# Performance work log

Hardware: AMD Instinct MI355X
Metric: run time of the kernel (lower is better)

Reference implementation:

```python
import jax, jax.numpy as jnp
import numpy as np
import math

B, N, HID, NH = 128, 512, 512, 8
DH = HID // NH  # d_heads = 64


def setup_inputs() -> dict:
    key = jax.random.key(0)
    ks = jax.random.split(key, 8)
    s = 0.05  # keep logits in a sane range
    h = jax.random.normal(ks[0], (B, N, HID), dtype=jnp.float32)
    lengths = jax.random.randint(ks[1], (B,), 1, N + 1, dtype=jnp.int32)
    w_q = jax.random.normal(ks[2], (HID, HID), dtype=jnp.float32) * s
    w_k = jax.random.normal(ks[3], (HID, HID), dtype=jnp.float32) * s
    w_v = jax.random.normal(ks[4], (HID, HID), dtype=jnp.float32) * s
    w_o = jax.random.normal(ks[5], (HID, HID), dtype=jnp.float32) * s
    w_seed_w = jax.random.normal(ks[6], (HID, 1), dtype=jnp.float32) * s  # Linear(1, k*hidden), k=1
    w_seed_b = jax.random.normal(ks[7], (HID,), dtype=jnp.float32) * s
    seed_vec = jnp.ones((1,), dtype=jnp.float32)
    return {"h": h, "lengths": lengths, "w_q": w_q, "w_k": w_k, "w_v": w_v,
            "w_o": w_o, "w_seed_w": w_seed_w, "w_seed_b": w_seed_b, "seed_vec": seed_vec}


def reference(h, lengths, w_q, w_k, w_v, w_o, w_seed_w, w_seed_b, seed_vec):
    # PMA with k=1 seed query. norm_features=False.
    # query = w_seed(seed_vec), same for every graph in the batch.
    query = w_seed_w @ seed_vec + w_seed_b            # [HID]
    q = (w_q @ query).reshape(NH, DH)                 # [NH, DH] (Linear: x @ W.T == W @ x for vector)
    # NOTE: original code computes w_k(v) but never uses it in attention; output
    # depends only on q and v (e = q * v summed over d_heads). We skip the dead compute.
    v = (h @ w_v.T).reshape(B, N, NH, DH)             # [B, N, NH, DH]
    # logits: e[b,h,n] = <q[h], v[b,n,h]> / sqrt(DH)
    e = jnp.einsum("hd,bnhd->bhn", q, v) / math.sqrt(DH)
    valid = jnp.arange(N)[None, :] < lengths[:, None]  # [B, N] ragged mask
    e = jnp.where(valid[:, None, :], e, -jnp.inf)
    alpha = jax.nn.softmax(e, axis=-1)                # [B, NH, N]; padded cols -> 0
    out_h = jnp.einsum("bhn,bnhd->bhd", alpha, v)     # [B, NH, DH]
    out = out_h.reshape(B, HID) @ w_o.T               # [B*k, HID], packed (k=1)
    alpha_out = alpha[..., None]                      # [B, NH, N, 1] matching torch permute
    return out, alpha_out
```

## Files before the change

### kernel.cpp

```cpp
#include <hip/hip_runtime.h>
#include <math.h>

constexpr int B = 128, N = 512, HID = 512, NH = 8, DH = 64;

__global__ __launch_bounds__(64) void k1_qk(
    const float* __restrict__ w_q, const float* __restrict__ w_v,
    const float* __restrict__ w_sw, const float* __restrict__ w_sb,
    const float* __restrict__ seed, float* __restrict__ qk)
{
    __shared__ __align__(16) float query_s[HID];
    __shared__ float q_s[DH];
    const int t  = threadIdx.x;
    const int h  = blockIdx.x >> 3;
    const int jc = blockIdx.x & 7;
    const float sv = seed[0];
    #pragma unroll
    for (int k = 0; k < 8; ++k) {
        const int j = t * 8 + k;
        query_s[j] = w_sw[j] * sv + w_sb[j];
    }
    __syncthreads();
    {
        const float* row = w_q + (size_t)(h * DH + t) * HID;
        float acc = 0.f;
        for (int j = 0; j < HID; j += 4) {
            const float4 wv = *(const float4*)(row + j);
            acc += wv.x * query_s[j]     + wv.y * query_s[j + 1]
                 + wv.z * query_s[j + 2] + wv.w * query_s[j + 3];
        }
        q_s[t] = acc;
    }
    __syncthreads();
    {
        const int j = jc * 64 + t;
        float acc = 0.f;
        for (int d = 0; d < DH; ++d)
            acc += q_s[d] * w_v[(size_t)(h * DH + d) * HID + j];
        qk[h * HID + j] = acc * 0.125f;
    }
}

__global__ __launch_bounds__(256) void ke_logits(
    const float* __restrict__ hbuf, const int* __restrict__ lengths,
    const float* __restrict__ qk, float* __restrict__ e_ws)
{
    const int t = threadIdx.x;
    const int l = t & 63;
    const int w = t >> 6;
    const int b = blockIdx.x >> 3;
    const int c = blockIdx.x & 7;
    const int n0 = c * 64;
    const int len = lengths[b];
    if (n0 >= len) return;

    float4 qlo[NH], qhi[NH];
    #pragma unroll
    for (int hh = 0; hh < NH; ++hh) {
        qlo[hh] = *(const float4*)&qk[hh * HID + l * 4];
        qhi[hh] = *(const float4*)&qk[hh * HID + 256 + l * 4];
    }

    const int nmax = min(n0 + 64, len);
    const float* hb = hbuf + (size_t)b * N * HID;
    const int hh_out = ((l & 1) << 2) | (l & 2) | ((l >> 2) & 1);

    for (int n = n0 + w; n < nmax; n += 4) {
        const float* row = hb + (size_t)n * HID;
        const float4 h0 = *(const float4*)(row + l * 4);
        const float4 h1 = *(const float4*)(row + 256 + l * 4);
        float v[NH];
        #pragma unroll
        for (int hh = 0; hh < NH; ++hh)
            v[hh] = h0.x * qlo[hh].x + h0.y * qlo[hh].y
                  + h0.z * qlo[hh].z + h0.w * qlo[hh].w
                  + h1.x * qhi[hh].x + h1.y * qhi[hh].y
                  + h1.z * qhi[hh].z + h1.w * qhi[hh].w;

        #pragma unroll
        for (int i = 0; i < 4; ++i) {
            const float ax = __shfl_xor(v[i], 1, 64);
            const float bx = __shfl_xor(v[i + 4], 1, 64);
            v[i] = (l & 1) ? (v[i + 4] + bx) : (v[i] + ax);
        }
        #pragma unroll
        for (int i = 0; i < 2; ++i) {
            const float ax = __shfl_xor(v[i], 2, 64);
            const float bx = __shfl_xor(v[i + 2], 2, 64);
            v[i] = (l & 2) ? (v[i + 2] + bx) : (v[i] + ax);
        }
        {
            const float ax = __shfl_xor(v[0], 4, 64);
            const float bx = __shfl_xor(v[1], 4, 64);
            v[0] = (l & 4) ? (v[1] + bx) : (v[0] + ax);
        }
        v[0] += __shfl_xor(v[0], 8, 64);
        v[0] += __shfl_xor(v[0], 16, 64);
        v[0] += __shfl_xor(v[0], 32, 64);

        if (l < 8)
            e_ws[(size_t)(b * NH + hh_out) * N + n] = v[0];
    }
}

__global__ __launch_bounds__(256) void ks_softmax(
    const float* __restrict__ e_ws, const int* __restrict__ lengths,
    float* __restrict__ alpha, float* __restrict__ al_t)
{
    const int b    = blockIdx.x >> 1;
    const int grp  = blockIdx.x & 1;
    const int lane = threadIdx.x & 63;
    const int hh   = grp * 4 + (threadIdx.x >> 6);
    const int len  = lengths[b];

    const float* e = e_ws + (size_t)(b * NH + hh) * N;
    float ev[8];
    float m = -3.0e38f;
    #pragma unroll
    for (int it = 0; it < 8; ++it) {
        const int n = it * 64 + lane;
        ev[it] = (n < len) ? e[n] : -3.0e38f;
        m = fmaxf(m, ev[it]);
    }
    #pragma unroll
    for (int off = 32; off; off >>= 1)
        m = fmaxf(m, __shfl_xor(m, off, 64));
    float s = 0.f;
    #pragma unroll
    for (int it = 0; it < 8; ++it) {
        ev[it] = __expf(ev[it] - m);
        s += ev[it];
    }
    #pragma unroll
    for (int off = 32; off; off >>= 1)
        s += __shfl_xor(s, off, 64);
    const float inv = 1.f / s;
    float* ao = alpha + (size_t)(b * NH + hh) * N;
    float* at = al_t + (size_t)b * N * NH + hh;
    #pragma unroll
    for (int it = 0; it < 8; ++it) {
        const int n   = it * 64 + lane;
        const float v = (n < len) ? ev[it] * inv : 0.f;
        ao[n]      = v;
        at[n * NH] = v;
    }
}

__global__ __launch_bounds__(256) void kc_ctx(
    const float* __restrict__ hbuf, const int* __restrict__ lengths,
    const float* __restrict__ al_t, float* __restrict__ ctxp)
{
    __shared__ __align__(16) float4 red[NH][128];
    const int t   = threadIdx.x;
    const int b   = blockIdx.x >> 3;
    const int c   = blockIdx.x & 7;
    const int n0  = c * 64;
    const int g   = t >> 7;
    const int cq  = t & 127;
    const int len = lengths[b];
    const int nend = min(len - n0, 64);

    float4 acc[NH];
    #pragma unroll
    for (int hh = 0; hh < NH; ++hh) { acc[hh].x = acc[hh].y = acc[hh].z = acc[hh].w = 0.f; }

    const float* hb = hbuf + ((size_t)b * N + n0) * HID + cq * 4;
    const float* ap = al_t + ((size_t)b * N + n0) * NH;
    #pragma unroll 4
    for (int ln = g; ln < nend; ln += 2) {
        const float4 hv = *(const float4*)(hb + (size_t)ln * HID);
        const float* a = ap + ln * NH;
        acc[0].x += a[0] * hv.x; acc[0].y += a[0] * hv.y; acc[0].z += a[0] * hv.z; acc[0].w += a[0] * hv.w;
        acc[1].x += a[1] * hv.x; acc[1].y += a[1] * hv.y; acc[1].z += a[1] * hv.z; acc[1].w += a[1] * hv.w;
        acc[2].x += a[2] * hv.x; acc[2].y += a[2] * hv.y; acc[2].z += a[2] * hv.z; acc[2].w += a[2] * hv.w;
        acc[3].x += a[3] * hv.x; acc[3].y += a[3] * hv.y; acc[3].z += a[3] * hv.z; acc[3].w += a[3] * hv.w;
        acc[4].x += a[4] * hv.x; acc[4].y += a[4] * hv.y; acc[4].z += a[4] * hv.z; acc[4].w += a[4] * hv.w;
        acc[5].x += a[5] * hv.x; acc[5].y += a[5] * hv.y; acc[5].z += a[5] * hv.z; acc[5].w += a[5] * hv.w;
        acc[6].x += a[6] * hv.x; acc[6].y += a[6] * hv.y; acc[6].z += a[6] * hv.z; acc[6].w += a[6] * hv.w;
        acc[7].x += a[7] * hv.x; acc[7].y += a[7] * hv.y; acc[7].z += a[7] * hv.z; acc[7].w += a[7] * hv.w;
    }
    if (g == 1) {
        #pragma unroll
        for (int hh = 0; hh < NH; ++hh) red[hh][cq] = acc[hh];
    }
    __syncthreads();
    if (g == 0) {
        float* cp = ctxp + (size_t)((b * 8 + c) * NH) * HID + cq * 4;
        #pragma unroll
        for (int hh = 0; hh < NH; ++hh) {
            const float4 r = red[hh][cq];
            float4 o;
            o.x = acc[hh].x + r.x; o.y = acc[hh].y + r.y;
            o.z = acc[hh].z + r.z; o.w = acc[hh].w + r.w;
            *(float4*)(cp + (size_t)hh * HID) = o;
        }
    }
}

__global__ __launch_bounds__(256) void kd1_oh(
    const float* __restrict__ ctxp, const float* __restrict__ w_v,
    float* __restrict__ oh)
{
    __shared__ __align__(16) float ctx_s[16][HID];
    const int t  = threadIdx.x;
    const int ht = blockIdx.x & 7;
    const int bt = blockIdx.x >> 3;

    for (int idx = t; idx < 16 * 128; idx += 256) {
        const int bb_l = idx >> 7;
        const int j4   = idx & 127;
        const int bb   = bt * 16 + bb_l;
        const float* p0 = ctxp + ((size_t)(bb * 8) * NH + ht) * HID + j4 * 4;
        float4 s = {0.f, 0.f, 0.f, 0.f};
        #pragma unroll
        for (int cc = 0; cc < 8; ++cc) {
            const float4 v = *(const float4*)(p0 + (size_t)cc * NH * HID);
            s.x += v.x; s.y += v.y; s.z += v.z; s.w += v.w;
        }
        *(float4*)&ctx_s[bb_l][j4 * 4] = s;
    }
    __syncthreads();

    const int d  = t & 63;
    const int bs = t >> 6;
    const int p  = ht * 64 + d;
    const float* wrow = w_v + (size_t)p * HID;
    float acc[4] = {0.f, 0.f, 0.f, 0.f};
    for (int j = 0; j < HID; j += 4) {
        const float4 wv = *(const float4*)(wrow + j);
        #pragma unroll
        for (int bi = 0; bi < 4; ++bi) {
            const float4 cv = *(const float4*)&ctx_s[bs * 4 + bi][j];
            acc[bi] += wv.x * cv.x + wv.y * cv.y + wv.z * cv.z + wv.w * cv.w;
        }
    }
    #pragma unroll
    for (int bi = 0; bi < 4; ++bi) {
        const int bb = bt * 16 + bs * 4 + bi;
        oh[(size_t)bb * HID + p] = acc[bi];
    }
}

__global__ __launch_bounds__(256) void kd2_out(
    const float* __restrict__ oh, const float* __restrict__ w_o,
    float* __restrict__ out)
{
    __shared__ __align__(16) float oh_s[16][HID];
    const int t  = threadIdx.x;
    const int it = blockIdx.x & 7;
    const int bt = blockIdx.x >> 3;

    for (int idx = t; idx < 16 * 128; idx += 256) {
        const int bb_l = idx >> 7;
        const int j4   = idx & 127;
        const int bb   = bt * 16 + bb_l;
        *(float4*)&oh_s[bb_l][j4 * 4] =
            *(const float4*)&oh[(size_t)bb * HID + j4 * 4];
    }
    __syncthreads();

    const int d  = t & 63;
    const int bs = t >> 6;
    const int i  = it * 64 + d;
    const float* wrow = w_o + (size_t)i * HID;
    float acc[4] = {0.f, 0.f, 0.f, 0.f};
    for (int j = 0; j < HID; j += 4) {
        const float4 wv = *(const float4*)(wrow + j);
        #pragma unroll
        for (int bi = 0; bi < 4; ++bi) {
            const float4 ov = *(const float4*)&oh_s[bs * 4 + bi][j];
            acc[bi] += wv.x * ov.x + wv.y * ov.y + wv.z * ov.z + wv.w * ov.w;
        }
    }
    #pragma unroll
    for (int bi = 0; bi < 4; ++bi) {
        const int bb = bt * 16 + bs * 4 + bi;
        out[(size_t)bb * HID + i] = acc[bi];
    }
}

extern "C" void kernel_launch(void* const* d_in, const int* in_sizes, int n_in,
                              void* d_out, int out_size, void* d_ws, size_t ws_size,
                              hipStream_t stream) {
    const float* h     = (const float*)d_in[0];
    const int*   lens  = (const int*)  d_in[1];
    const float* w_q   = (const float*)d_in[2];
    const float* w_v   = (const float*)d_in[4];
    const float* w_o   = (const float*)d_in[5];
    const float* w_sw  = (const float*)d_in[6];
    const float* w_sb  = (const float*)d_in[7];
    const float* seed  = (const float*)d_in[8];

    float* out   = (float*)d_out;
    float* alpha = out + (size_t)B * HID;

    float* ws   = (float*)d_ws;
    float* qk   = ws;
    float* e_ws = qk + NH * HID;
    float* al_t = e_ws + (size_t)B * NH * N;
    float* ctxp = al_t + (size_t)B * N * NH;
    float* oh   = ctxp + (size_t)B * 8 * NH * HID;

    hipLaunchKernelGGL(k1_qk,      dim3(64),    dim3(64),  0, stream,
                       w_q, w_v, w_sw, w_sb, seed, qk);
    hipLaunchKernelGGL(ke_logits,  dim3(B * 8), dim3(256), 0, stream,
                       h, lens, qk, e_ws);
    hipLaunchKernelGGL(ks_softmax, dim3(B * 2), dim3(256), 0, stream,
                       e_ws, lens, alpha, al_t);
    hipLaunchKernelGGL(kc_ctx,     dim3(B * 8), dim3(256), 0, stream,
                       h, lens, al_t, ctxp);
    hipLaunchKernelGGL(kd1_oh,     dim3(64),    dim3(256), 0, stream,
                       ctxp, w_v, oh);
    hipLaunchKernelGGL(kd2_out,    dim3(64),    dim3(256), 0, stream,
                       oh, w_o, out);
}
```

Measured before the change: 291.0 us.

## Fuse softmax into context kernel with transposed logits layout

```diff
diff --git a/kernel.cpp b/kernel.cpp
--- a/kernel.cpp
+++ b/kernel.cpp
@@ -42,7 +42,7 @@
 
 __global__ __launch_bounds__(256) void ke_logits(
     const float* __restrict__ hbuf, const int* __restrict__ lengths,
-    const float* __restrict__ qk, float* __restrict__ e_ws)
+    const float* __restrict__ qk, float* __restrict__ e_t)
 {
     const int t = threadIdx.x;
     const int l = t & 63;
@@ -98,65 +98,93 @@
         v[0] += __shfl_xor(v[0], 32, 64);
 
         if (l < 8)
-            e_ws[(size_t)(b * NH + hh_out) * N + n] = v[0];
-    }
-}
-
-__global__ __launch_bounds__(256) void ks_softmax(
-    const float* __restrict__ e_ws, const int* __restrict__ lengths,
-    float* __restrict__ alpha, float* __restrict__ al_t)
-{
-    const int b    = blockIdx.x >> 1;
-    const int grp  = blockIdx.x & 1;
-    const int lane = threadIdx.x & 63;
-    const int hh   = grp * 4 + (threadIdx.x >> 6);
-    const int len  = lengths[b];
-
-    const float* e = e_ws + (size_t)(b * NH + hh) * N;
-    float ev[8];
-    float m = -3.0e38f;
-    #pragma unroll
-    for (int it = 0; it < 8; ++it) {
-        const int n = it * 64 + lane;
-        ev[it] = (n < len) ? e[n] : -3.0e38f;
-        m = fmaxf(m, ev[it]);
-    }
-    #pragma unroll
-    for (int off = 32; off; off >>= 1)
-        m = fmaxf(m, __shfl_xor(m, off, 64));
-    float s = 0.f;
-    #pragma unroll
-    for (int it = 0; it < 8; ++it) {
-        ev[it] = __expf(ev[it] - m);
-        s += ev[it];
-    }
-    #pragma unroll
-    for (int off = 32; off; off >>= 1)
-        s += __shfl_xor(s, off, 64);
-    const float inv = 1.f / s;
-    float* ao = alpha + (size_t)(b * NH + hh) * N;
-    float* at = al_t + (size_t)b * N * NH + hh;
-    #pragma unroll
-    for (int it = 0; it < 8; ++it) {
-        const int n   = it * 64 + lane;
-        const float v = (n < len) ? ev[it] * inv : 0.f;
-        ao[n]      = v;
-        at[n * NH] = v;
-    }
-}
-
-__global__ __launch_bounds__(256) void kc_ctx(
+            e_t[((size_t)b * N + n) * NH + hh_out] = v[0];
+    }
+}
+
+__global__ __launch_bounds__(256) void kcs_ctx(
     const float* __restrict__ hbuf, const int* __restrict__ lengths,
-    const float* __restrict__ al_t, float* __restrict__ ctxp)
-{
-    __shared__ __align__(16) float4 red[NH][128];
-    const int t   = threadIdx.x;
-    const int b   = blockIdx.x >> 3;
-    const int c   = blockIdx.x & 7;
-    const int n0  = c * 64;
-    const int g   = t >> 7;
-    const int cq  = t & 127;
+    const float* __restrict__ e_t, float* __restrict__ alpha,
+    float* __restrict__ ctxp)
+{
+    __shared__ float red_s[NH][256];
+    __shared__ float stat_s[2][NH];
+    __shared__ __align__(16) float al_s[64][8];
+    __shared__ __align__(16) float4 red4[NH][128];
+    const int t = threadIdx.x;
+    const int l = t & 63;
+    const int w = t >> 6;
+    const int b = blockIdx.x >> 3;
+    const int c = blockIdx.x & 7;
+    const int n0 = c * 64;
     const int len = lengths[b];
+
+    const float* eb = e_t + (size_t)b * N * NH;
+    float4 ev[4];
+    {
+        const float4* ep = (const float4*)(eb + t * 16);
+        ev[0] = ep[0]; ev[1] = ep[1]; ev[2] = ep[2]; ev[3] = ep[3];
+    }
+    const bool va = (2 * t) < len, vb = (2 * t + 1) < len;
+    const float* e0 = (const float*)&ev[0];
+    const float* e1 = (const float*)&ev[2];
+    #pragma unroll
+    for (int hh = 0; hh < NH; ++hh) {
+        float m = -3.0e38f;
+        if (va) m = e0[hh];
+        if (vb) m = fmaxf(m, e1[hh]);
+        red_s[hh][t] = m;
+    }
+    __syncthreads();
+    #pragma unroll
+    for (int k = 0; k < 2; ++k) {
+        const int hh = w + k * 4;
+        float v = fmaxf(fmaxf(red_s[hh][l], red_s[hh][l + 64]),
+                        fmaxf(red_s[hh][l + 128], red_s[hh][l + 192]));
+        #pragma unroll
+        for (int off = 32; off; off >>= 1)
+            v = fmaxf(v, __shfl_xor(v, off, 64));
+        if (l == 0) stat_s[0][hh] = v;
+    }
+    __syncthreads();
+
+    #pragma unroll
+    for (int hh = 0; hh < NH; ++hh) {
+        const float m = stat_s[0][hh];
+        float s = 0.f;
+        if (va) s += __expf(e0[hh] - m);
+        if (vb) s += __expf(e1[hh] - m);
+        red_s[hh][t] = s;
+    }
+    __syncthreads();
+    #pragma unroll
+    for (int k = 0; k < 2; ++k) {
+        const int hh = w + k * 4;
+        float v = red_s[hh][l] + red_s[hh][l + 64]
+                + red_s[hh][l + 128] + red_s[hh][l + 192];
+        #pragma unroll
+        for (int off = 32; off; off >>= 1)
+            v += __shfl_xor(v, off, 64);
+        if (l == 0) stat_s[1][hh] = 1.f / v;
+    }
+    __syncthreads();
+
+    #pragma unroll
+    for (int k = 0; k < 2; ++k) {
+        const int idx = t + k * 256;
+        const int hh = idx >> 6;
+        const int nl = idx & 63;
+        const int n  = n0 + nl;
+        float v = 0.f;
+        if (n < len)
+            v = __expf(eb[(size_t)n * NH + hh] - stat_s[0][hh]) * stat_s[1][hh];
+        alpha[(size_t)(b * NH + hh) * N + n] = v;
+        al_s[nl][hh] = v;
+    }
+    __syncthreads();
+
+    const int g  = t >> 7;
+    const int cq = t & 127;
     const int nend = min(len - n0, 64);
 
     float4 acc[NH];
@@ -164,30 +192,30 @@
     for (int hh = 0; hh < NH; ++hh) { acc[hh].x = acc[hh].y = acc[hh].z = acc[hh].w = 0.f; }
 
     const float* hb = hbuf + ((size_t)b * N + n0) * HID + cq * 4;
-    const float* ap = al_t + ((size_t)b * N + n0) * NH;
     #pragma unroll 4
     for (int ln = g; ln < nend; ln += 2) {
         const float4 hv = *(const float4*)(hb + (size_t)ln * HID);
-        const float* a = ap + ln * NH;
-        acc[0].x += a[0] * hv.x; acc[0].y += a[0] * hv.y; acc[0].z += a[0] * hv.z; acc[0].w += a[0] * hv.w;
-        acc[1].x += a[1] * hv.x; acc[1].y += a[1] * hv.y; acc[1].z += a[1] * hv.z; acc[1].w += a[1] * hv.w;
-        acc[2].x += a[2] * hv.x; acc[2].y += a[2] * hv.y; acc[2].z += a[2] * hv.z; acc[2].w += a[2] * hv.w;
-        acc[3].x += a[3] * hv.x; acc[3].y += a[3] * hv.y; acc[3].z += a[3] * hv.z; acc[3].w += a[3] * hv.w;
-        acc[4].x += a[4] * hv.x; acc[4].y += a[4] * hv.y; acc[4].z += a[4] * hv.z; acc[4].w += a[4] * hv.w;
-        acc[5].x += a[5] * hv.x; acc[5].y += a[5] * hv.y; acc[5].z += a[5] * hv.z; acc[5].w += a[5] * hv.w;
-        acc[6].x += a[6] * hv.x; acc[6].y += a[6] * hv.y; acc[6].z += a[6] * hv.z; acc[6].w += a[6] * hv.w;
-        acc[7].x += a[7] * hv.x; acc[7].y += a[7] * hv.y; acc[7].z += a[7] * hv.z; acc[7].w += a[7] * hv.w;
+        const float4 a0 = *(const float4*)&al_s[ln][0];
+        const float4 a1 = *(const float4*)&al_s[ln][4];
+        acc[0].x += a0.x * hv.x; acc[0].y += a0.x * hv.y; acc[0].z += a0.x * hv.z; acc[0].w += a0.x * hv.w;
+        acc[1].x += a0.y * hv.x; acc[1].y += a0.y * hv.y; acc[1].z += a0.y * hv.z; acc[1].w += a0.y * hv.w;
+        acc[2].x += a0.z * hv.x; acc[2].y += a0.z * hv.y; acc[2].z += a0.z * hv.z; acc[2].w += a0.z * hv.w;
+        acc[3].x += a0.w * hv.x; acc[3].y += a0.w * hv.y; acc[3].z += a0.w * hv.z; acc[3].w += a0.w * hv.w;
+        acc[4].x += a1.x * hv.x; acc[4].y += a1.x * hv.y; acc[4].z += a1.x * hv.z; acc[4].w += a1.x * hv.w;
+        acc[5].x += a1.y * hv.x; acc[5].y += a1.y * hv.y; acc[5].z += a1.y * hv.z; acc[5].w += a1.y * hv.w;
+        acc[6].x += a1.z * hv.x; acc[6].y += a1.z * hv.y; acc[6].z += a1.z * hv.z; acc[6].w += a1.z * hv.w;
+        acc[7].x += a1.w * hv.x; acc[7].y += a1.w * hv.y; acc[7].z += a1.w * hv.z; acc[7].w += a1.w * hv.w;
     }
     if (g == 1) {
         #pragma unroll
-        for (int hh = 0; hh < NH; ++hh) red[hh][cq] = acc[hh];
+        for (int hh = 0; hh < NH; ++hh) red4[hh][cq] = acc[hh];
     }
     __syncthreads();
     if (g == 0) {
         float* cp = ctxp + (size_t)((b * 8 + c) * NH) * HID + cq * 4;
         #pragma unroll
         for (int hh = 0; hh < NH; ++hh) {
-            const float4 r = red[hh][cq];
+            const float4 r = red4[hh][cq];
             float4 o;
             o.x = acc[hh].x + r.x; o.y = acc[hh].y + r.y;
             o.z = acc[hh].z + r.z; o.w = acc[hh].w + r.w;
@@ -295,21 +323,18 @@
 
     float* ws   = (float*)d_ws;
     float* qk   = ws;
-    float* e_ws = qk + NH * HID;
-    float* al_t = e_ws + (size_t)B * NH * N;
-    float* ctxp = al_t + (size_t)B * N * NH;
+    float* e_t  = qk + NH * HID;
+    float* ctxp = e_t + (size_t)B * N * NH;
     float* oh   = ctxp + (size_t)B * 8 * NH * HID;
 
-    hipLaunchKernelGGL(k1_qk,      dim3(64),    dim3(64),  0, stream,
+    hipLaunchKernelGGL(k1_qk,     dim3(64),    dim3(64),  0, stream,
                        w_q, w_v, w_sw, w_sb, seed, qk);
-    hipLaunchKernelGGL(ke_logits,  dim3(B * 8), dim3(256), 0, stream,
-                       h, lens, qk, e_ws);
-    hipLaunchKernelGGL(ks_softmax, dim3(B * 2), dim3(256), 0, stream,
-                       e_ws, lens, alpha, al_t);
-    hipLaunchKernelGGL(kc_ctx,     dim3(B * 8), dim3(256), 0, stream,
-                       h, lens, al_t, ctxp);
-    hipLaunchKernelGGL(kd1_oh,     dim3(64),    dim3(256), 0, stream,
+    hipLaunchKernelGGL(ke_logits, dim3(B * 8), dim3(256), 0, stream,
+                       h, lens, qk, e_t);
+    hipLaunchKernelGGL(kcs_ctx,   dim3(B * 8), dim3(256), 0, stream,
+                       h, lens, e_t, alpha, ctxp);
+    hipLaunchKernelGGL(kd1_oh,    dim3(64),    dim3(256), 0, stream,
                        ctxp, w_v, oh);
-    hipLaunchKernelGGL(kd2_out,    dim3(64),    dim3(256), 0, stream,
+    hipLaunchKernelGGL(kd2_out,   dim3(64),    dim3(256), 0, stream,
                        oh, w_o, out);
 }
```

New measurement: 280.6 us. 3.6% less time.
